# Kernel optimization log

Hardware: AMD Instinct MI355X
Metric: run time of the kernel (lower is better)

The kernel has to match this reference:

```python
import jax, jax.numpy as jnp
import numpy as np

WS = 14            # window side (14x14 patches)
DIM = 768          # model dim (ViT-Base)
H = 12             # heads
HD = DIM // H      # head dim = 64
B = 128            # batch
N = WS * WS + 1    # 197 tokens (patches + CLS)
NRD = (2 * WS - 1) ** 2 + 3  # num_relative_distance = 732


def _rel_index():
    # Faithful replication of the torch buffer construction.
    coords = np.stack(np.meshgrid(np.arange(WS), np.arange(WS), indexing='ij'))  # [2,WS,WS]
    flat = coords.reshape(2, -1)                                   # [2, WS*WS]
    rel = flat[:, :, None] - flat[:, None, :]                      # [2, P, P]
    rel = rel.transpose(1, 2, 0).astype(np.int64)                  # [P, P, 2]
    rel[:, :, 0] += WS - 1
    rel[:, :, 1] += WS - 1
    rel[:, :, 0] *= 2 * WS - 1
    idx = np.zeros((N, N), dtype=np.int64)
    idx[1:, 1:] = rel.sum(-1)
    idx[0, :] = NRD - 3
    idx[:, 0] = NRD - 2
    idx[0, 0] = NRD - 1
    return jnp.asarray(idx, dtype=jnp.int32)


def setup_inputs() -> dict:
    key = jax.random.key(0)
    ks = jax.random.split(key, 5)
    return {
        'x': jax.random.normal(ks[0], (B, N, DIM), dtype=jnp.float32),
        'qkv_w': jax.random.normal(ks[1], (3 * DIM, DIM), dtype=jnp.float32) * 0.02,
        'q_bias': jnp.zeros((DIM,), jnp.float32),
        'v_bias': jnp.zeros((DIM,), jnp.float32),
        'rpb_table': jax.random.normal(ks[2], (NRD, H), dtype=jnp.float32) * 0.02,
        'proj_w': jax.random.normal(ks[3], (DIM, DIM), dtype=jnp.float32) * 0.02,
        'proj_b': jnp.zeros((DIM,), jnp.float32),
        'rel_idx': _rel_index(),
    }


def reference(x, qkv_w, q_bias, v_bias, rpb_table, proj_w, proj_b, rel_idx):
    Bv, Nv, C = x.shape
    scale = HD ** -0.5
    # qkv_bias = cat(q_bias, zeros, v_bias); eval mode so dropout is identity
    bias = jnp.concatenate([q_bias, jnp.zeros_like(v_bias), v_bias])
    qkv = x @ qkv_w.T + bias                                   # [B,N,3*DIM]
    qkv = qkv.reshape(Bv, Nv, 3, H, HD).transpose(2, 0, 3, 1, 4)
    q, k, v = qkv[0] * scale, qkv[1], qkv[2]                   # [B,H,N,HD]
    attn = jnp.einsum('bhqd,bhkd->bhqk', q, k)                 # [B,H,N,N]
    rpb = rpb_table[rel_idx]                                   # gather -> [N,N,H]
    attn = attn + rpb.transpose(2, 0, 1)[None]                 # + [1,H,N,N]
    attn = jax.nn.softmax(attn, axis=-1)
    out = jnp.einsum('bhqk,bhkd->bhqd', attn, v)               # [B,H,N,HD]
    out = out.transpose(0, 2, 1, 3).reshape(Bv, Nv, H * HD)
    return out @ proj_w.T + proj_b
```

## Files before the change

kernel.cpp:

```cpp
#include <hip/hip_runtime.h>
#include <hip/hip_bf16.h>
#include <cstdint>

#define BATCH 128
#define NTOK  197
#define NHEAD 12

typedef __attribute__((ext_vector_type(8))) __bf16 bf16x8;
typedef __attribute__((ext_vector_type(4))) float f32x4;
typedef __attribute__((ext_vector_type(4))) unsigned short ushort4v;

#define KSTR 72

__device__ __forceinline__ unsigned short f2bf(float f) {
    union { float f; unsigned int u; } v; v.f = f;
    unsigned int r = (v.u + 0x7FFFu + ((v.u >> 16) & 1u)) >> 16;
    return (unsigned short)r;
}

__device__ __forceinline__ void async_cp16(const void* gsrc, void* lds_dst) {
    __builtin_amdgcn_global_load_lds(
        (const __attribute__((address_space(1))) unsigned int*)((uintptr_t)gsrc),
        (__attribute__((address_space(3))) unsigned int*)((uintptr_t)lds_dst),
        16, 0, 0);
}

__global__ void bias_tiles(const float* __restrict__ rpb,
                           const int* __restrict__ rel_idx,
                           float* __restrict__ BT) {
    int idx = blockIdx.x * 256 + threadIdx.x;
    int r    = idx & 3;
    int j    = (idx >> 2) & 3;
    int l16  = (idx >> 4) & 15;
    int quad = (idx >> 8) & 3;
    int kt   = (idx >> 10) & 3;
    int qt   = (idx >> 12) & 15;
    int h    = idx >> 16;
    int qn = qt * 16 + quad * 4 + r; if (qn > 196) qn = 196;
    int kn = kt * 64 + j * 16 + l16;
    float v = 0.f;
    if (kn < NTOK) v = rpb[rel_idx[qn * NTOK + kn] * NHEAD + h];
    BT[idx] = v;
}

__global__ __launch_bounds__(256) void cvt_bf16(const float4* __restrict__ src,
                                                ushort4v* __restrict__ dst, int n4) {
    int i = blockIdx.x * 256 + threadIdx.x;
    if (i >= n4) return;
    float4 f = src[i];
    ushort4v o;
    o.x = f2bf(f.x); o.y = f2bf(f.y); o.z = f2bf(f.z); o.w = f2bf(f.w);
    dst[i] = o;
}

template <int EPI>
__global__ __launch_bounds__(256) void gemm_mfma(
    const unsigned short* __restrict__ A,
    const unsigned short* __restrict__ W,
    const float* __restrict__ bias1, const float* __restrict__ bias2,
    unsigned short* __restrict__ oq, unsigned short* __restrict__ ok,
    unsigned short* __restrict__ ov, float* __restrict__ outf,
    int Mc) {
    __shared__ unsigned short As[128 * 32];
    __shared__ unsigned short Bs[128 * 32];

    const int t    = threadIdx.x;
    const int lane = t & 63;
    const int wave = t >> 6;
    const int wm   = wave >> 1;
    const int wn   = wave & 1;
    const int quad = lane >> 4;
    const int l16  = lane & 15;
    const int m0   = blockIdx.y * 128;
    const int n0   = blockIdx.x * 128;

    const int srow = lane >> 2;
    const int scol = (lane & 3) * 8;
    int ar0 = m0 + wave * 32 + srow;      if (ar0 >= Mc) ar0 = Mc - 1;
    int ar1 = m0 + wave * 32 + 16 + srow; if (ar1 >= Mc) ar1 = Mc - 1;
    const unsigned short* Ag0 = A + (size_t)ar0 * 768 + scol;
    const unsigned short* Ag1 = A + (size_t)ar1 * 768 + scol;
    const unsigned short* Wg0 = W + (size_t)(n0 + wave * 32 + srow) * 768 + scol;
    const unsigned short* Wg1 = Wg0 + (size_t)16 * 768;
    unsigned short* Ad0 = As + (wave * 32) * 32;
    unsigned short* Ad1 = As + (wave * 32 + 16) * 32;
    unsigned short* Bd0 = Bs + (wave * 32) * 32;
    unsigned short* Bd1 = Bs + (wave * 32 + 16) * 32;

    const unsigned short* Afp = As + (wm * 64 + l16) * 32 + quad * 8;
    const unsigned short* Bfp = Bs + (wn * 64 + l16) * 32 + quad * 8;

    f32x4 acc[4][4] = {};

    for (int k0 = 0; k0 < 768; k0 += 32) {
        __syncthreads();
        async_cp16(Ag0 + k0, Ad0);
        async_cp16(Ag1 + k0, Ad1);
        async_cp16(Wg0 + k0, Bd0);
        async_cp16(Wg1 + k0, Bd1);
        __syncthreads();
        bf16x8 af[4], bfr[4];
#pragma unroll
        for (int i = 0; i < 4; i++) af[i]  = *(const bf16x8*)(Afp + i * 16 * 32);
#pragma unroll
        for (int j = 0; j < 4; j++) bfr[j] = *(const bf16x8*)(Bfp + j * 16 * 32);
#pragma unroll
        for (int i = 0; i < 4; i++)
#pragma unroll
            for (int j = 0; j < 4; j++)
                acc[i][j] = __builtin_amdgcn_mfma_f32_16x16x32_bf16(
                    af[i], bfr[j], acc[i][j], 0, 0, 0);
    }

    if (EPI == 0) {
        const int part   = n0 / 768;
        const float scale = (part == 0) ? 0.125f : 1.f;
        unsigned short* dst = (part == 0) ? oq : (part == 1 ? ok : ov);
        const int nb0 = n0 - part * 768;
#pragma unroll
        for (int j = 0; j < 4; j++) {
            const int nnb = nb0 + wn * 64 + j * 16;
            const int h   = nnb >> 6;
            const int d   = (nnb & 63) + l16;
            const float bb = (part == 0) ? bias1[nnb + l16]
                           : (part == 2 ? bias2[nnb + l16] : 0.f);
#pragma unroll
            for (int i = 0; i < 4; i++) {
                const int mb = m0 + wm * 64 + i * 16 + quad * 4;
#pragma unroll
                for (int r = 0; r < 4; r++) {
                    const int m = mb + r;
                    if (m < Mc) {
                        const int bi  = m / NTOK;
                        const int tok = m - bi * NTOK;
                        dst[(((size_t)bi * NHEAD + h) * NTOK + tok) * 64 + d] =
                            f2bf((acc[i][j][r] + bb) * scale);
                    }
                }
            }
        }
    } else {
#pragma unroll
        for (int j = 0; j < 4; j++) {
            const int col = n0 + wn * 64 + j * 16 + l16;
            const float bb = bias1[col];
#pragma unroll
            for (int i = 0; i < 4; i++) {
                const int mb = m0 + wm * 64 + i * 16 + quad * 4;
#pragma unroll
                for (int r = 0; r < 4; r++) {
                    const int m = mb + r;
                    if (m < Mc) outf[(size_t)m * 768 + col] = acc[i][j][r] + bb;
                }
            }
        }
    }
}

__global__ __launch_bounds__(256, 2) void attn_mfma(
    const unsigned short* __restrict__ Q, const unsigned short* __restrict__ K,
    const unsigned short* __restrict__ V, const float* __restrict__ BT,
    unsigned short* __restrict__ AO) {
    __shared__ unsigned short Ks[64 * KSTR];
    __shared__ unsigned short Vt[64 * KSTR];
    __shared__ unsigned short Ps[4][64 * KSTR];

    const int t    = threadIdx.x;
    const int lane = t & 63;
    const int wave = t >> 6;
    const int quad = lane >> 4;
    const int l16  = lane & 15;
    const int bh   = blockIdx.x;
    const int b    = bh / NHEAD;
    const int h    = bh - b * NHEAD;

    const unsigned short* qb = Q + (size_t)bh * NTOK * 64;
    const unsigned short* kb = K + (size_t)bh * NTOK * 64;
    const unsigned short* vb = V + (size_t)bh * NTOK * 64;

    bf16x8 qf[4][2];
#pragma unroll
    for (int i = 0; i < 4; i++) {
        int tok = wave * 64 + i * 16 + l16; if (tok > 196) tok = 196;
#pragma unroll
        for (int ks = 0; ks < 2; ks++)
            qf[i][ks] = *(const bf16x8*)&qb[(size_t)tok * 64 + ks * 32 + quad * 8];
    }

    f32x4 O[4][4] = {};
    float lsum[4][4] = {};

    for (int kt = 0; kt < 4; kt++) {
        __syncthreads();
        {
            const int row = t >> 2, cg = t & 3;
            int gk = kt * 64 + row; if (gk > 196) gk = 196;
            const uint4* src = (const uint4*)&kb[(size_t)gk * 64 + cg * 16];
            *(uint4*)&Ks[row * KSTR + cg * 16]     = src[0];
            *(uint4*)&Ks[row * KSTR + cg * 16 + 8] = src[1];
        }
        {
            const int key = t & 63, dg = t >> 6;
            int gk = kt * 64 + key; if (gk > 196) gk = 196;
            union { uint4 v4[2]; unsigned short u[16]; } tmp;
            const uint4* src = (const uint4*)&vb[(size_t)gk * 64 + dg * 16];
            tmp.v4[0] = src[0]; tmp.v4[1] = src[1];
#pragma unroll
            for (int u = 0; u < 16; u++) Vt[(dg * 16 + u) * KSTR + key] = tmp.u[u];
        }
        __syncthreads();

        f32x4 acc[4][4];
#pragma unroll
        for (int i = 0; i < 4; i++) {
            const float4* bp = (const float4*)&BT[
                (((((size_t)h * 16 + (wave * 4 + i)) * 4 + kt) * 4 + quad) * 16 + l16) * 16];
#pragma unroll
            for (int j = 0; j < 4; j++) {
                float4 f = bp[j];
                acc[i][j] = (f32x4){f.x, f.y, f.z, f.w};
            }
        }

#pragma unroll
        for (int ks = 0; ks < 2; ks++) {
            bf16x8 kf[4];
#pragma unroll
            for (int j = 0; j < 4; j++)
                kf[j] = *(const bf16x8*)&Ks[(j * 16 + l16) * KSTR + ks * 32 + quad * 8];
#pragma unroll
            for (int i = 0; i < 4; i++)
#pragma unroll
                for (int j = 0; j < 4; j++)
                    acc[i][j] = __builtin_amdgcn_mfma_f32_16x16x32_bf16(
                        qf[i][ks], kf[j], acc[i][j], 0, 0, 0);
        }

#pragma unroll
        for (int j = 0; j < 4; j++) {
            const int kn = kt * 64 + j * 16 + l16;
            const bool kval = (kn < NTOK);
#pragma unroll
            for (int i = 0; i < 4; i++)
#pragma unroll
                for (int r = 0; r < 4; r++) {
                    float p = kval ? __expf(fminf(acc[i][j][r], 30.f)) : 0.f;
                    lsum[i][r] += p;
                    Ps[wave][(i * 16 + quad * 4 + r) * KSTR + j * 16 + l16] = f2bf(p);
                }
        }

#pragma unroll
        for (int ks = 0; ks < 2; ks++) {
            bf16x8 vf[4], pf[4];
#pragma unroll
            for (int jd = 0; jd < 4; jd++)
                vf[jd] = *(const bf16x8*)&Vt[(jd * 16 + l16) * KSTR + ks * 32 + quad * 8];
#pragma unroll
            for (int i = 0; i < 4; i++)
                pf[i] = *(const bf16x8*)&Ps[wave][(i * 16 + l16) * KSTR + ks * 32 + quad * 8];
#pragma unroll
            for (int i = 0; i < 4; i++)
#pragma unroll
                for (int jd = 0; jd < 4; jd++)
                    O[i][jd] = __builtin_amdgcn_mfma_f32_16x16x32_bf16(
                        pf[i], vf[jd], O[i][jd], 0, 0, 0);
        }
    }

#pragma unroll
    for (int i = 0; i < 4; i++)
#pragma unroll
        for (int r = 0; r < 4; r++) {
            float l = lsum[i][r];
            l += __shfl_xor(l, 1); l += __shfl_xor(l, 2);
            l += __shfl_xor(l, 4); l += __shfl_xor(l, 8);
            lsum[i][r] = 1.f / l;
        }
#pragma unroll
    for (int i = 0; i < 4; i++) {
        const int tb = wave * 64 + i * 16 + quad * 4;
#pragma unroll
        for (int r = 0; r < 4; r++) {
            const int tok = tb + r;
            if (tok < NTOK) {
                const float rl = lsum[i][r];
#pragma unroll
                for (int jd = 0; jd < 4; jd++)
                    AO[((size_t)b * NTOK + tok) * 768 + h * 64 + jd * 16 + l16] =
                        f2bf(O[i][jd][r] * rl);
            }
        }
    }
}

extern "C" void kernel_launch(void* const* d_in, const int* in_sizes, int n_in,
                              void* d_out, int out_size, void* d_ws, size_t ws_size,
                              hipStream_t stream) {
    const float* x      = (const float*)d_in[0];
    const float* qkv_w  = (const float*)d_in[1];
    const float* q_bias = (const float*)d_in[2];
    const float* v_bias = (const float*)d_in[3];
    const float* rpb    = (const float*)d_in[4];
    const float* proj_w = (const float*)d_in[5];
    const float* proj_b = (const float*)d_in[6];
    const int*   rel_idx = (const int*)d_in[7];
    float* out = (float*)d_out;

    const size_t EB   = 151296;
    const size_t NBT  = 786432;
    const size_t NX   = (size_t)BATCH * NTOK * 768;
    const size_t NWQ  = (size_t)2304 * 768;
    const size_t NWP  = (size_t)768 * 768;

    const size_t fixed_bytes = NBT * 4 + (NX + NWQ + NWP) * 2;
    int Bc = BATCH;
    while (Bc > 1 && fixed_bytes + 8ull * Bc * EB > ws_size) Bc >>= 1;
    if (fixed_bytes + 8ull * Bc * EB > ws_size) return;
    const int nc = BATCH / Bc;
    const int Mc = Bc * NTOK;
    const int Gy = (Mc + 127) / 128;

    float* BT             = (float*)d_ws;
    unsigned short* xbf   = (unsigned short*)(BT + NBT);
    unsigned short* wqkv  = xbf + NX;
    unsigned short* wproj = wqkv + NWQ;
    unsigned short* q     = wproj + NWP;
    unsigned short* k     = q + (size_t)Bc * EB;
    unsigned short* v     = k + (size_t)Bc * EB;
    unsigned short* aobf  = v + (size_t)Bc * EB;

    bias_tiles<<<(int)(NBT / 256), 256, 0, stream>>>(rpb, rel_idx, BT);
    cvt_bf16<<<(int)((NX / 4 + 255) / 256), 256, 0, stream>>>(
        (const float4*)x, (ushort4v*)xbf, (int)(NX / 4));
    cvt_bf16<<<(int)((NWQ / 4 + 255) / 256), 256, 0, stream>>>(
        (const float4*)qkv_w, (ushort4v*)wqkv, (int)(NWQ / 4));
    cvt_bf16<<<(int)((NWP / 4 + 255) / 256), 256, 0, stream>>>(
        (const float4*)proj_w, (ushort4v*)wproj, (int)(NWP / 4));

    for (int c = 0; c < nc; c++) {
        gemm_mfma<0><<<dim3(2304 / 128, Gy), 256, 0, stream>>>(
            xbf + (size_t)c * Mc * 768, wqkv, q_bias, v_bias, q, k, v, nullptr, Mc);
        attn_mfma<<<Bc * NHEAD, 256, 0, stream>>>(q, k, v, BT, aobf);
        gemm_mfma<1><<<dim3(768 / 128, Gy), 256, 0, stream>>>(
            aobf, wproj, proj_b, nullptr, nullptr, nullptr, nullptr,
            out + (size_t)c * Mc * 768, Mc);
    }
}
```

Before: 472.7 us.

## Rewrite GEMM as 256x256 tile with double-buffered swizzled LDS and 8 waves

The GEMM kernel moves from 128x128 tiles with 4 waves and a single-buffered LDS stage to 256x256 tiles with 8 waves, a K step of 64, and two LDS buffers filled by async global-to-LDS copies. A prefetch of the next K slice overlaps the MFMA work, and an XOR swizzle on the LDS columns is meant to avoid bank conflicts. Explicit s_waitcnt, barriers, sched_barrier and setprio interleave the waves. This cuts global traffic per flop and hides load latency. The cost is 128 KB of LDS and large accumulator register pressure. The bigger tiles also give fewer blocks, which may leave CUs idle, especially for the 768-wide projection GEMM.

```diff
diff --git a/kernel.cpp b/kernel.cpp
--- a/kernel.cpp
+++ b/kernel.cpp
@@ -54,79 +54,114 @@
 }
 
 template <int EPI>
-__global__ __launch_bounds__(256) void gemm_mfma(
+__global__ __launch_bounds__(512, 2) void gemm_mfma(
     const unsigned short* __restrict__ A,
     const unsigned short* __restrict__ W,
     const float* __restrict__ bias1, const float* __restrict__ bias2,
     unsigned short* __restrict__ oq, unsigned short* __restrict__ ok,
     unsigned short* __restrict__ ov, float* __restrict__ outf,
     int Mc) {
-    __shared__ unsigned short As[128 * 32];
-    __shared__ unsigned short Bs[128 * 32];
+    __shared__ unsigned short lds[65536];
 
     const int t    = threadIdx.x;
     const int lane = t & 63;
     const int wave = t >> 6;
-    const int wm   = wave >> 1;
-    const int wn   = wave & 1;
+    const int wm   = wave >> 2;
+    const int wn   = wave & 3;
     const int quad = lane >> 4;
     const int l16  = lane & 15;
-    const int m0   = blockIdx.y * 128;
-    const int n0   = blockIdx.x * 128;
-
-    const int srow = lane >> 2;
-    const int scol = (lane & 3) * 8;
-    int ar0 = m0 + wave * 32 + srow;      if (ar0 >= Mc) ar0 = Mc - 1;
-    int ar1 = m0 + wave * 32 + 16 + srow; if (ar1 >= Mc) ar1 = Mc - 1;
-    const unsigned short* Ag0 = A + (size_t)ar0 * 768 + scol;
-    const unsigned short* Ag1 = A + (size_t)ar1 * 768 + scol;
-    const unsigned short* Wg0 = W + (size_t)(n0 + wave * 32 + srow) * 768 + scol;
-    const unsigned short* Wg1 = Wg0 + (size_t)16 * 768;
-    unsigned short* Ad0 = As + (wave * 32) * 32;
-    unsigned short* Ad1 = As + (wave * 32 + 16) * 32;
-    unsigned short* Bd0 = Bs + (wave * 32) * 32;
-    unsigned short* Bd1 = Bs + (wave * 32 + 16) * 32;
-
-    const unsigned short* Afp = As + (wm * 64 + l16) * 32 + quad * 8;
-    const unsigned short* Bfp = Bs + (wn * 64 + l16) * 32 + quad * 8;
-
-    f32x4 acc[4][4] = {};
-
-    for (int k0 = 0; k0 < 768; k0 += 32) {
-        __syncthreads();
-        async_cp16(Ag0 + k0, Ad0);
-        async_cp16(Ag1 + k0, Ad1);
-        async_cp16(Wg0 + k0, Bd0);
-        async_cp16(Wg1 + k0, Bd1);
-        __syncthreads();
-        bf16x8 af[4], bfr[4];
-#pragma unroll
-        for (int i = 0; i < 4; i++) af[i]  = *(const bf16x8*)(Afp + i * 16 * 32);
-#pragma unroll
-        for (int j = 0; j < 4; j++) bfr[j] = *(const bf16x8*)(Bfp + j * 16 * 32);
-#pragma unroll
-        for (int i = 0; i < 4; i++)
-#pragma unroll
-            for (int j = 0; j < 4; j++)
-                acc[i][j] = __builtin_amdgcn_mfma_f32_16x16x32_bf16(
-                    af[i], bfr[j], acc[i][j], 0, 0, 0);
+    const int m0   = blockIdx.y * 256;
+    const int n0   = blockIdx.x * 256;
+
+    const int srow = wave * 8 + (lane >> 3);
+    const int scol = (((lane & 7) ^ (lane >> 3)) << 3);
+    const unsigned short* Asrc[4];
+    const unsigned short* Wsrc[4];
+#pragma unroll
+    for (int l = 0; l < 4; l++) {
+        int ra = m0 + l * 64 + srow; if (ra >= Mc) ra = Mc - 1;
+        Asrc[l] = A + (size_t)ra * 768 + scol;
+        Wsrc[l] = W + (size_t)(n0 + l * 64 + srow) * 768 + scol;
+    }
+
+    auto stage = [&](int c, int kt) {
+        unsigned short* Ab = lds + c * 32768;
+        unsigned short* Bb = Ab + 16384;
+#pragma unroll
+        for (int l = 0; l < 4; l++) {
+            async_cp16(Asrc[l] + kt * 64, Ab + (l * 64 + wave * 8) * 64);
+            async_cp16(Wsrc[l] + kt * 64, Bb + (l * 64 + wave * 8) * 64);
+        }
+    };
+
+    const int arow0 = wm * 128 + l16;
+    const int brow0 = wn * 64 + l16;
+    const int csw0  = ((quad ^ (l16 & 7)) << 3);
+    const int csw1  = (((4 + quad) ^ (l16 & 7)) << 3);
+
+    f32x4 acc[8][4] = {};
+
+    stage(0, 0);
+#pragma unroll 1
+    for (int kt = 0; kt < 12; kt++) {
+        const int c = kt & 1;
+        if (kt < 11) {
+            stage(c ^ 1, kt + 1);
+            asm volatile("s_waitcnt vmcnt(8)" ::: "memory");
+        } else {
+            asm volatile("s_waitcnt vmcnt(0)" ::: "memory");
+        }
+        __builtin_amdgcn_s_barrier();
+        __builtin_amdgcn_sched_barrier(0);
+
+        const unsigned short* Ab = lds + c * 32768;
+        const unsigned short* Bb = Ab + 16384;
+
+        bf16x8 bfr[4][2];
+#pragma unroll
+        for (int nf = 0; nf < 4; nf++) {
+            bfr[nf][0] = *(const bf16x8*)(Bb + (brow0 + nf * 16) * 64 + csw0);
+            bfr[nf][1] = *(const bf16x8*)(Bb + (brow0 + nf * 16) * 64 + csw1);
+        }
+#pragma unroll
+        for (int p = 0; p < 4; p++) {
+            bf16x8 af[2][2];
+#pragma unroll
+            for (int i = 0; i < 2; i++) {
+                af[i][0] = *(const bf16x8*)(Ab + (arow0 + (p * 2 + i) * 16) * 64 + csw0);
+                af[i][1] = *(const bf16x8*)(Ab + (arow0 + (p * 2 + i) * 16) * 64 + csw1);
+            }
+            __builtin_amdgcn_s_barrier();
+            __builtin_amdgcn_sched_barrier(0);
+            __builtin_amdgcn_s_setprio(1);
+#pragma unroll
+            for (int kk = 0; kk < 2; kk++)
+#pragma unroll
+                for (int i = 0; i < 2; i++)
+#pragma unroll
+                    for (int nf = 0; nf < 4; nf++)
+                        acc[p * 2 + i][nf] = __builtin_amdgcn_mfma_f32_16x16x32_bf16(
+                            af[i][kk], bfr[nf][kk], acc[p * 2 + i][nf], 0, 0, 0);
+            __builtin_amdgcn_s_setprio(0);
+            __builtin_amdgcn_sched_barrier(0);
+            __builtin_amdgcn_s_barrier();
+        }
     }
 
     if (EPI == 0) {
         const int part   = n0 / 768;
         const float scale = (part == 0) ? 0.125f : 1.f;
         unsigned short* dst = (part == 0) ? oq : (part == 1 ? ok : ov);
-        const int nb0 = n0 - part * 768;
-#pragma unroll
-        for (int j = 0; j < 4; j++) {
-            const int nnb = nb0 + wn * 64 + j * 16;
-            const int h   = nnb >> 6;
-            const int d   = (nnb & 63) + l16;
-            const float bb = (part == 0) ? bias1[nnb + l16]
-                           : (part == 2 ? bias2[nnb + l16] : 0.f);
-#pragma unroll
-            for (int i = 0; i < 4; i++) {
-                const int mb = m0 + wm * 64 + i * 16 + quad * 4;
+        const int nb = (n0 - part * 768) + wn * 64;
+        const int h  = nb >> 6;
+#pragma unroll
+        for (int nf = 0; nf < 4; nf++) {
+            const int d = nf * 16 + l16;
+            const float bb = (part == 0) ? bias1[nb + nf * 16 + l16]
+                           : (part == 2 ? bias2[nb + nf * 16 + l16] : 0.f);
+#pragma unroll
+            for (int mf = 0; mf < 8; mf++) {
+                const int mb = m0 + wm * 128 + mf * 16 + quad * 4;
 #pragma unroll
                 for (int r = 0; r < 4; r++) {
                     const int m = mb + r;
@@ -134,23 +169,23 @@
                         const int bi  = m / NTOK;
                         const int tok = m - bi * NTOK;
                         dst[(((size_t)bi * NHEAD + h) * NTOK + tok) * 64 + d] =
-                            f2bf((acc[i][j][r] + bb) * scale);
+                            f2bf((acc[mf][nf][r] + bb) * scale);
                     }
                 }
             }
         }
     } else {
 #pragma unroll
-        for (int j = 0; j < 4; j++) {
-            const int col = n0 + wn * 64 + j * 16 + l16;
+        for (int nf = 0; nf < 4; nf++) {
+            const int col = n0 + wn * 64 + nf * 16 + l16;
             const float bb = bias1[col];
 #pragma unroll
-            for (int i = 0; i < 4; i++) {
-                const int mb = m0 + wm * 64 + i * 16 + quad * 4;
+            for (int mf = 0; mf < 8; mf++) {
+                const int mb = m0 + wm * 128 + mf * 16 + quad * 4;
 #pragma unroll
                 for (int r = 0; r < 4; r++) {
                     const int m = mb + r;
-                    if (m < Mc) outf[(size_t)m * 768 + col] = acc[i][j][r] + bb;
+                    if (m < Mc) outf[(size_t)m * 768 + col] = acc[mf][nf][r] + bb;
                 }
             }
         }
@@ -319,7 +354,7 @@
     if (fixed_bytes + 8ull * Bc * EB > ws_size) return;
     const int nc = BATCH / Bc;
     const int Mc = Bc * NTOK;
-    const int Gy = (Mc + 127) / 128;
+    const int Gy = (Mc + 255) / 256;
 
     float* BT             = (float*)d_ws;
     unsigned short* xbf   = (unsigned short*)(BT + NBT);
@@ -339,10 +374,10 @@
         (const float4*)proj_w, (ushort4v*)wproj, (int)(NWP / 4));
 
     for (int c = 0; c < nc; c++) {
-        gemm_mfma<0><<<dim3(2304 / 128, Gy), 256, 0, stream>>>(
+        gemm_mfma<0><<<dim3(2304 / 256, Gy), 512, 0, stream>>>(
             xbf + (size_t)c * Mc * 768, wqkv, q_bias, v_bias, q, k, v, nullptr, Mc);
         attn_mfma<<<Bc * NHEAD, 256, 0, stream>>>(q, k, v, BT, aobf);
-        gemm_mfma<1><<<dim3(768 / 128, Gy), 256, 0, stream>>>(
+        gemm_mfma<1><<<dim3(768 / 256, Gy), 512, 0, stream>>>(
             aobf, wproj, proj_b, nullptr, nullptr, nullptr, nullptr,
             out + (size_t)c * Mc * 768, Mc);
     }
```

After: 501.4 us. +6.1%, slower.
